# Performance work log

Hardware: AMD Instinct MI355X
Metric: run time of the kernel (lower is better)

Reference implementation:

```python
import jax, jax.numpy as jnp
import numpy as np

D_MODEL = 768
N_HEADS = 12
HEAD_DIM = D_MODEL // N_HEADS
D_FF = 3072
LN_EPS = 1e-12


def layer_norm(x, gamma, beta, eps=LN_EPS):
    mu = jnp.mean(x, axis=-1, keepdims=True)
    var = jnp.var(x, axis=-1, keepdims=True)
    return (x - mu) * jax.lax.rsqrt(var + eps) * gamma + beta


def setup_inputs() -> dict:
    key = jax.random.key(0)
    ks = jax.random.split(key, 16)
    B, S = 4, 2048
    p = lambda k, shape: (jax.random.normal(k, shape, dtype=jnp.float32) * 0.02)
    return {
        "hidden_states": jax.random.normal(ks[0], (B, S, D_MODEL), dtype=jnp.float32),
        "Wq": p(ks[1], (D_MODEL, D_MODEL)), "bq": jnp.zeros((D_MODEL,), jnp.float32),
        "Wk": p(ks[2], (D_MODEL, D_MODEL)), "bk": jnp.zeros((D_MODEL,), jnp.float32),
        "Wv": p(ks[3], (D_MODEL, D_MODEL)), "bv": jnp.zeros((D_MODEL,), jnp.float32),
        "Wo": p(ks[4], (D_MODEL, D_MODEL)), "bo": jnp.zeros((D_MODEL,), jnp.float32),
        "ln1_g": jnp.ones((D_MODEL,), jnp.float32), "ln1_b": jnp.zeros((D_MODEL,), jnp.float32),
        "Wi": p(ks[5], (D_FF, D_MODEL)), "bi": jnp.zeros((D_FF,), jnp.float32),
        "Wf": p(ks[6], (D_MODEL, D_FF)), "bf": jnp.zeros((D_MODEL,), jnp.float32),
        "ln2_g": jnp.ones((D_MODEL,), jnp.float32), "ln2_b": jnp.zeros((D_MODEL,), jnp.float32),
    }


def reference(hidden_states, Wq, bq, Wk, bk, Wv, bv, Wo, bo, ln1_g, ln1_b,
              Wi, bi, Wf, bf, ln2_g, ln2_b):
    B, S, _ = hidden_states.shape
    # Q/K/V projections (computed as in source; outputs then overwritten by constants)
    q = hidden_states @ Wq.T + bq
    k = hidden_states @ Wk.T + bk
    v = hidden_states @ Wv.T + bv
    split = lambda x: x.reshape(B, S, N_HEADS, HEAD_DIM).transpose(0, 2, 1, 3)
    q, k, v = split(q), split(k), split(v)
    # source: torch.full_like(..., 0.01) overwrite of q/k/v
    q = jnp.full_like(q, 0.01)
    k = jnp.full_like(k, 0.01)
    v = jnp.full_like(v, 0.01)
    # naive attention: full [B,H,S,S] score matrix materialized
    scores = jnp.einsum("bhqd,bhkd->bhqk", q, k) / jnp.sqrt(jnp.float32(HEAD_DIM))
    probs = jax.nn.softmax(scores, axis=-1)
    ctx = jnp.einsum("bhqk,bhkd->bhqd", probs, v)
    ctx = ctx.transpose(0, 2, 1, 3).reshape(B, S, D_MODEL)
    # self-output: dense + residual + LayerNorm (dropout is identity in eval)
    attn_out = layer_norm(ctx @ Wo.T + bo + hidden_states, ln1_g, ln1_b)
    # FFN: fc1 + exact GELU, fc2 + residual + LayerNorm
    h = jax.nn.gelu(attn_out @ Wi.T + bi, approximate=False)
    layer_out = layer_norm(h @ Wf.T + bf + attn_out, ln2_g, ln2_b)
    return layer_out
```

## Files before the change

kernel.cpp:

```cpp
#include <hip/hip_runtime.h>
#include <hip/hip_bf16.h>
#include <cstdint>
#include <cstddef>


typedef __bf16 bf16;
typedef __attribute__((ext_vector_type(8))) __bf16 bf16x8;
typedef __attribute__((ext_vector_type(4))) __bf16 bf16x4;
typedef __attribute__((ext_vector_type(4))) float floatx4;

#define DM    768
#define DF    3072
#define MROWS 8192

#define N8          (DF * DM / 8)
#define CONV_BLOCKS (2 * N8 / 256)
#define CVEC_BLOCKS (DM / 4)

__device__ __forceinline__ void gl2lds16(const void* gp, void* lp) {
  __builtin_amdgcn_global_load_lds(
      (__attribute__((address_space(1))) void*)(void*)gp,
      (__attribute__((address_space(3))) void*)lp,
      16, 0, 0);
}

__device__ __forceinline__ float gelu_fast(float x) {
  float x2 = x * x;
  float m  = x * __builtin_fmaf(-0.1029641f, x2, -2.3025851f);
  float e  = __builtin_amdgcn_exp2f(m);
  return x * __builtin_amdgcn_rcpf(1.0f + e);
}

__global__ __launch_bounds__(256)
void prep_kernel(const float* __restrict__ Wi, const float* __restrict__ Wf,
                 bf16* __restrict__ Wib, bf16* __restrict__ Wfb,
                 const float* __restrict__ Wo, const float* __restrict__ bo,
                 float* __restrict__ cvec) {
  if (blockIdx.x < CONV_BLOCKS) {
    int i = blockIdx.x * 256 + threadIdx.x;
    const float* src = (i < N8) ? Wi : Wf;
    bf16* dst        = (i < N8) ? Wib : Wfb;
    int k            = (i < N8) ? i : i - N8;
    const float4* p = (const float4*)(src + (size_t)k * 8);
    float4 x = p[0], y = p[1];
    bf16x8 o;
    o[0]=(bf16)x.x; o[1]=(bf16)x.y; o[2]=(bf16)x.z; o[3]=(bf16)x.w;
    o[4]=(bf16)y.x; o[5]=(bf16)y.y; o[6]=(bf16)y.z; o[7]=(bf16)y.w;
    *(bf16x8*)(dst + (size_t)k * 8) = o;
  } else {
    int row  = (blockIdx.x - CONV_BLOCKS) * 4 + (threadIdx.x >> 6);
    int lane = threadIdx.x & 63;
    const float4* r = (const float4*)(Wo + (size_t)row * DM);
    float s = 0.f;
    #pragma unroll
    for (int t = 0; t < 3; ++t) {
      float4 v = r[lane + t * 64];
      s += v.x + v.y + v.z + v.w;
    }
    #pragma unroll
    for (int o = 32; o > 0; o >>= 1) s += __shfl_xor(s, o);
    if (lane == 0) cvec[row] = 0.01f * s + bo[row];
  }
}

__global__ __launch_bounds__(256)
void ln1_kernel(const float* __restrict__ hid, const float* __restrict__ cvec,
                const float* __restrict__ g, const float* __restrict__ b,
                bf16* __restrict__ out) {
  int row  = blockIdx.x * 4 + (threadIdx.x >> 6);
  int lane = threadIdx.x & 63;
  const float4* hrow = (const float4*)(hid + (size_t)row * DM);
  const float4* cv4  = (const float4*)cvec;
  float x[12];
  float s = 0.f, sq = 0.f;
  #pragma unroll
  for (int t = 0; t < 3; ++t) {
    int c = lane + t * 64;
    float4 v = hrow[c];
    float4 cc = cv4[c];
    float x0 = v.x + cc.x, x1 = v.y + cc.y, x2 = v.z + cc.z, x3 = v.w + cc.w;
    x[t*4+0] = x0; x[t*4+1] = x1; x[t*4+2] = x2; x[t*4+3] = x3;
    s  += x0 + x1 + x2 + x3;
    sq += x0*x0 + x1*x1 + x2*x2 + x3*x3;
  }
  #pragma unroll
  for (int o = 32; o > 0; o >>= 1) { s += __shfl_xor(s, o); sq += __shfl_xor(sq, o); }
  float mu  = s * (1.0f / DM);
  float var = sq * (1.0f / DM) - mu * mu;
  float inv = rsqrtf(var + 1e-12f);
  const float4* g4 = (const float4*)g;
  const float4* b4 = (const float4*)b;
  #pragma unroll
  for (int t = 0; t < 3; ++t) {
    int c = lane + t * 64;
    float4 gg = g4[c], bb = b4[c];
    bf16x4 o4;
    o4[0] = (bf16)((x[t*4+0] - mu) * inv * gg.x + bb.x);
    o4[1] = (bf16)((x[t*4+1] - mu) * inv * gg.y + bb.y);
    o4[2] = (bf16)((x[t*4+2] - mu) * inv * gg.z + bb.z);
    o4[3] = (bf16)((x[t*4+3] - mu) * inv * gg.w + bb.w);
    *(bf16x4*)(out + (size_t)row * DM + c * 4) = o4;
  }
}

__global__ __launch_bounds__(256)
void ln2_kernel(const bf16* __restrict__ p0, const bf16* __restrict__ p1,
                const float* __restrict__ bias, const bf16* __restrict__ attn,
                const float* __restrict__ g, const float* __restrict__ b,
                float* __restrict__ out) {
  int row  = blockIdx.x * 4 + (threadIdx.x >> 6);
  int lane = threadIdx.x & 63;
  const bf16* r0 = p0 + (size_t)row * DM;
  const bf16* r1 = p1 + (size_t)row * DM;
  const bf16* ar = attn + (size_t)row * DM;
  const float4* bi4 = (const float4*)bias;
  float x[12];
  float s = 0.f, sq = 0.f;
  #pragma unroll
  for (int t = 0; t < 3; ++t) {
    int c = lane + t * 64;
    bf16x4 a = *(const bf16x4*)(r0 + c * 4);
    bf16x4 d = *(const bf16x4*)(r1 + c * 4);
    bf16x4 rv = *(const bf16x4*)(ar + c * 4);
    float4 bb = bi4[c];
    float x0 = (float)a[0] + (float)d[0] + bb.x + (float)rv[0];
    float x1 = (float)a[1] + (float)d[1] + bb.y + (float)rv[1];
    float x2 = (float)a[2] + (float)d[2] + bb.z + (float)rv[2];
    float x3 = (float)a[3] + (float)d[3] + bb.w + (float)rv[3];
    x[t*4+0] = x0; x[t*4+1] = x1; x[t*4+2] = x2; x[t*4+3] = x3;
    s  += x0 + x1 + x2 + x3;
    sq += x0*x0 + x1*x1 + x2*x2 + x3*x3;
  }
  #pragma unroll
  for (int o = 32; o > 0; o >>= 1) { s += __shfl_xor(s, o); sq += __shfl_xor(sq, o); }
  float mu  = s * (1.0f / DM);
  float var = sq * (1.0f / DM) - mu * mu;
  float inv = rsqrtf(var + 1e-12f);
  const float4* g4 = (const float4*)g;
  const float4* b4 = (const float4*)b;
  float4* orow = (float4*)(out + (size_t)row * DM);
  #pragma unroll
  for (int t = 0; t < 3; ++t) {
    int c = lane + t * 64;
    float4 gg = g4[c], bb = b4[c];
    float4 o;
    o.x = (x[t*4+0] - mu) * inv * gg.x + bb.x;
    o.y = (x[t*4+1] - mu) * inv * gg.y + bb.y;
    o.z = (x[t*4+2] - mu) * inv * gg.z + bb.z;
    o.w = (x[t*4+3] - mu) * inv * gg.w + bb.w;
    orow[c] = o;
  }
}

#define BM 128
#define BN 128
#define BK 64
#define ES 136

template <int EPI>
__global__ __launch_bounds__(256)
void gemm_nt(const bf16* __restrict__ A, const bf16* __restrict__ B,
             const float* __restrict__ bias,
             bf16* __restrict__ out, int M, int N, int K, int ksplit) {
  __shared__ __align__(16) unsigned char smem[BM * ES * 2];
  bf16* lds_a = (bf16*)smem;
  bf16* lds_b = lds_a + BM * BK;

  const int tid   = threadIdx.x;
  const int wave  = tid >> 6;
  const int lane  = tid & 63;
  const int quad  = lane >> 4;
  const int row16 = lane & 15;
  const int xorv  = row16 & 7;

  const int m0 = blockIdx.y * BM;
  const int n0 = blockIdx.x * BN;
  const int wm = (wave >> 1) * 64;
  const int wn = (wave & 1) * 64;

  const int kbeg = blockIdx.z * ksplit;
  const int kend = kbeg + ksplit;

  floatx4 acc[4][4] = {};

  const bf16* Ablk = A + (size_t)m0 * K;
  const bf16* Bblk = B + (size_t)n0 * K;

  for (int kk = kbeg; kk < kend; kk += BK) {
    #pragma unroll
    for (int i = 0; i < 4; ++i) {
      int ci  = tid + 256 * i;
      int r   = ci >> 3;
      int c_g = (ci & 7) ^ (r & 7);
      gl2lds16(Ablk + (size_t)r * K + kk + c_g * 8, lds_a + ci * 8);
      gl2lds16(Bblk + (size_t)r * K + kk + c_g * 8, lds_b + ci * 8);
    }
    __syncthreads();

    #pragma unroll
    for (int ks = 0; ks < BK; ks += 32) {
      const int cs = ((ks >> 3) + quad) ^ xorv;
      bf16x8 af[4], bfr[4];
      #pragma unroll
      for (int i = 0; i < 4; ++i)
        af[i] = *(const bf16x8*)&lds_a[(wm + i * 16 + row16) * BK + cs * 8];
      #pragma unroll
      for (int j = 0; j < 4; ++j)
        bfr[j] = *(const bf16x8*)&lds_b[(wn + j * 16 + row16) * BK + cs * 8];
      #pragma unroll
      for (int i = 0; i < 4; ++i)
        #pragma unroll
        for (int j = 0; j < 4; ++j)
          acc[i][j] = __builtin_amdgcn_mfma_f32_16x16x32_bf16(af[i], bfr[j], acc[i][j], 0, 0, 0);
    }
    __syncthreads();
  }

  bf16* eb = (bf16*)smem;

  float bia[4];
  if constexpr (EPI == 0) {
    #pragma unroll
    for (int j = 0; j < 4; ++j) bia[j] = bias[n0 + wn + j * 16 + row16];
  }

  #pragma unroll
  for (int i = 0; i < 4; ++i) {
    #pragma unroll
    for (int j = 0; j < 4; ++j) {
      int col = wn + j * 16 + row16;
      #pragma unroll
      for (int r = 0; r < 4; ++r) {
        int row = wm + i * 16 + quad * 4 + r;
        float x = acc[i][j][r];
        if constexpr (EPI == 0) x = gelu_fast(x + bia[j]);
        eb[row * ES + col] = (bf16)x;
      }
    }
  }
  __syncthreads();

  bf16* outp = out + (EPI == 1 ? (size_t)blockIdx.z * M * N : 0);
  const int rsub = tid >> 4;
  const int csub = (tid & 15) * 8;
  #pragma unroll
  for (int c = 0; c < 8; ++c) {
    int row = c * 16 + rsub;
    bf16x8 v = *(const bf16x8*)&eb[row * ES + csub];
    *(bf16x8*)&outp[(size_t)(m0 + row) * N + n0 + csub] = v;
  }
}

extern "C" void kernel_launch(void* const* d_in, const int* in_sizes, int n_in,
                              void* d_out, int out_size, void* d_ws, size_t ws_size,
                              hipStream_t stream) {
  (void)in_sizes; (void)n_in; (void)out_size; (void)ws_size;

  const float* hidden = (const float*)d_in[0];
  const float* Wo     = (const float*)d_in[7];
  const float* bo     = (const float*)d_in[8];
  const float* ln1_g  = (const float*)d_in[9];
  const float* ln1_b  = (const float*)d_in[10];
  const float* Wi     = (const float*)d_in[11];
  const float* bi     = (const float*)d_in[12];
  const float* Wf     = (const float*)d_in[13];
  const float* bf_    = (const float*)d_in[14];
  const float* ln2_g  = (const float*)d_in[15];
  const float* ln2_b  = (const float*)d_in[16];
  float* out = (float*)d_out;

  char* w = (char*)d_ws;
  float* cvec = (float*)w;
  size_t off = 4096;
  bf16* attn = (bf16*)(w + off); off += (size_t)MROWS * DM * 2;
  bf16* h    = (bf16*)(w + off); off += (size_t)MROWS * DF * 2;
  bf16* pre  = (bf16*)(w + off); off += (size_t)2 * MROWS * DM * 2;
  bf16* Wib  = (bf16*)(w + off); off += (size_t)DF * DM * 2;
  bf16* Wfb  = (bf16*)(w + off);

  prep_kernel<<<dim3(CONV_BLOCKS + CVEC_BLOCKS), dim3(256), 0, stream>>>(
      Wi, Wf, Wib, Wfb, Wo, bo, cvec);

  ln1_kernel<<<dim3(MROWS / 4), dim3(256), 0, stream>>>(hidden, cvec, ln1_g, ln1_b, attn);

  gemm_nt<0><<<dim3(DF / BN, MROWS / BM, 1), dim3(256), 0, stream>>>(
      attn, Wib, bi, h, MROWS, DF, DM, DM);

  gemm_nt<1><<<dim3(DM / BN, MROWS / BM, 2), dim3(256), 0, stream>>>(
      h, Wfb, nullptr, pre, MROWS, DM, DF, DF / 2);

  ln2_kernel<<<dim3(MROWS / 4), dim3(256), 0, stream>>>(
      pre, pre + (size_t)MROWS * DM, bf_, attn, ln2_g, ln2_b, out);
}
```

Measured before the change: 238.4 us.

## Fuse LayerNorm2 into split-K FC2 GEMM via last-block atomic election

Removes the separate ln2 kernel launch. Each FC2 GEMM block writes its bf16 partial tile and increments a per-row-block atomic counter. The block that sees the final count (12 tiles: 6 N-tiles times 2 K-splits) then runs LayerNorm over that 128-row slab. The counter is zeroed in the prep kernel. This saves a launch and lets the LN overlap with GEMM tail work, but the LN is now serialized onto one block per row slab, which may leave CUs idle at the end.

```diff
diff --git a/kernel.cpp b/kernel.cpp
--- a/kernel.cpp
+++ b/kernel.cpp
@@ -35,7 +35,7 @@
 void prep_kernel(const float* __restrict__ Wi, const float* __restrict__ Wf,
                  bf16* __restrict__ Wib, bf16* __restrict__ Wfb,
                  const float* __restrict__ Wo, const float* __restrict__ bo,
-                 float* __restrict__ cvec) {
+                 float* __restrict__ cvec, int* __restrict__ ctr) {
   if (blockIdx.x < CONV_BLOCKS) {
     int i = blockIdx.x * 256 + threadIdx.x;
     const float* src = (i < N8) ? Wi : Wf;
@@ -48,6 +48,8 @@
     o[4]=(bf16)y.x; o[5]=(bf16)y.y; o[6]=(bf16)y.z; o[7]=(bf16)y.w;
     *(bf16x8*)(dst + (size_t)k * 8) = o;
   } else {
+    if (blockIdx.x == CONV_BLOCKS && threadIdx.x < 64)
+      ctr[threadIdx.x] = 0;
     int row  = (blockIdx.x - CONV_BLOCKS) * 4 + (threadIdx.x >> 6);
     int lane = threadIdx.x & 63;
     const float4* r = (const float4*)(Wo + (size_t)row * DM);
@@ -103,65 +105,15 @@
   }
 }
 
-__global__ __launch_bounds__(256)
-void ln2_kernel(const bf16* __restrict__ p0, const bf16* __restrict__ p1,
-                const float* __restrict__ bias, const bf16* __restrict__ attn,
-                const float* __restrict__ g, const float* __restrict__ b,
-                float* __restrict__ out) {
-  int row  = blockIdx.x * 4 + (threadIdx.x >> 6);
-  int lane = threadIdx.x & 63;
-  const bf16* r0 = p0 + (size_t)row * DM;
-  const bf16* r1 = p1 + (size_t)row * DM;
-  const bf16* ar = attn + (size_t)row * DM;
-  const float4* bi4 = (const float4*)bias;
-  float x[12];
-  float s = 0.f, sq = 0.f;
-  #pragma unroll
-  for (int t = 0; t < 3; ++t) {
-    int c = lane + t * 64;
-    bf16x4 a = *(const bf16x4*)(r0 + c * 4);
-    bf16x4 d = *(const bf16x4*)(r1 + c * 4);
-    bf16x4 rv = *(const bf16x4*)(ar + c * 4);
-    float4 bb = bi4[c];
-    float x0 = (float)a[0] + (float)d[0] + bb.x + (float)rv[0];
-    float x1 = (float)a[1] + (float)d[1] + bb.y + (float)rv[1];
-    float x2 = (float)a[2] + (float)d[2] + bb.z + (float)rv[2];
-    float x3 = (float)a[3] + (float)d[3] + bb.w + (float)rv[3];
-    x[t*4+0] = x0; x[t*4+1] = x1; x[t*4+2] = x2; x[t*4+3] = x3;
-    s  += x0 + x1 + x2 + x3;
-    sq += x0*x0 + x1*x1 + x2*x2 + x3*x3;
-  }
-  #pragma unroll
-  for (int o = 32; o > 0; o >>= 1) { s += __shfl_xor(s, o); sq += __shfl_xor(sq, o); }
-  float mu  = s * (1.0f / DM);
-  float var = sq * (1.0f / DM) - mu * mu;
-  float inv = rsqrtf(var + 1e-12f);
-  const float4* g4 = (const float4*)g;
-  const float4* b4 = (const float4*)b;
-  float4* orow = (float4*)(out + (size_t)row * DM);
-  #pragma unroll
-  for (int t = 0; t < 3; ++t) {
-    int c = lane + t * 64;
-    float4 gg = g4[c], bb = b4[c];
-    float4 o;
-    o.x = (x[t*4+0] - mu) * inv * gg.x + bb.x;
-    o.y = (x[t*4+1] - mu) * inv * gg.y + bb.y;
-    o.z = (x[t*4+2] - mu) * inv * gg.z + bb.z;
-    o.w = (x[t*4+3] - mu) * inv * gg.w + bb.w;
-    orow[c] = o;
-  }
-}
-
 #define BM 128
 #define BN 128
 #define BK 64
 #define ES 136
 
-template <int EPI>
 __global__ __launch_bounds__(256)
-void gemm_nt(const bf16* __restrict__ A, const bf16* __restrict__ B,
-             const float* __restrict__ bias,
-             bf16* __restrict__ out, int M, int N, int K, int ksplit) {
+void gemm1(const bf16* __restrict__ A, const bf16* __restrict__ B,
+           const float* __restrict__ bias, bf16* __restrict__ out,
+           int M, int N, int K) {
   __shared__ __align__(16) unsigned char smem[BM * ES * 2];
   bf16* lds_a = (bf16*)smem;
   bf16* lds_b = lds_a + BM * BK;
@@ -178,15 +130,11 @@
   const int wm = (wave >> 1) * 64;
   const int wn = (wave & 1) * 64;
 
-  const int kbeg = blockIdx.z * ksplit;
-  const int kend = kbeg + ksplit;
-
   floatx4 acc[4][4] = {};
-
   const bf16* Ablk = A + (size_t)m0 * K;
   const bf16* Bblk = B + (size_t)n0 * K;
 
-  for (int kk = kbeg; kk < kend; kk += BK) {
+  for (int kk = 0; kk < K; kk += BK) {
     #pragma unroll
     for (int i = 0; i < 4; ++i) {
       int ci  = tid + 256 * i;
@@ -196,7 +144,6 @@
       gl2lds16(Bblk + (size_t)r * K + kk + c_g * 8, lds_b + ci * 8);
     }
     __syncthreads();
-
     #pragma unroll
     for (int ks = 0; ks < BK; ks += 32) {
       const int cs = ((ks >> 3) + quad) ^ xorv;
@@ -217,30 +164,106 @@
   }
 
   bf16* eb = (bf16*)smem;
-
   float bia[4];
-  if constexpr (EPI == 0) {
-    #pragma unroll
-    for (int j = 0; j < 4; ++j) bia[j] = bias[n0 + wn + j * 16 + row16];
-  }
-
-  #pragma unroll
-  for (int i = 0; i < 4; ++i) {
+  #pragma unroll
+  for (int j = 0; j < 4; ++j) bia[j] = bias[n0 + wn + j * 16 + row16];
+
+  #pragma unroll
+  for (int i = 0; i < 4; ++i)
     #pragma unroll
     for (int j = 0; j < 4; ++j) {
       int col = wn + j * 16 + row16;
       #pragma unroll
       for (int r = 0; r < 4; ++r) {
         int row = wm + i * 16 + quad * 4 + r;
-        float x = acc[i][j][r];
-        if constexpr (EPI == 0) x = gelu_fast(x + bia[j]);
-        eb[row * ES + col] = (bf16)x;
+        eb[row * ES + col] = (bf16)gelu_fast(acc[i][j][r] + bia[j]);
       }
     }
-  }
   __syncthreads();
 
-  bf16* outp = out + (EPI == 1 ? (size_t)blockIdx.z * M * N : 0);
+  const int rsub = tid >> 4;
+  const int csub = (tid & 15) * 8;
+  #pragma unroll
+  for (int c = 0; c < 8; ++c) {
+    int row = c * 16 + rsub;
+    bf16x8 v = *(const bf16x8*)&eb[row * ES + csub];
+    *(bf16x8*)&out[(size_t)(m0 + row) * N + n0 + csub] = v;
+  }
+}
+
+__global__ __launch_bounds__(256)
+void gemm2_ln(const bf16* __restrict__ A, const bf16* __restrict__ B,
+              bf16* __restrict__ partial, const bf16* __restrict__ attn,
+              const float* __restrict__ bias,
+              const float* __restrict__ g, const float* __restrict__ b,
+              float* __restrict__ out, int* __restrict__ ctr) {
+  const int M = MROWS, N = DM, K = DF;
+  __shared__ __align__(16) unsigned char smem[BM * ES * 2];
+  bf16* lds_a = (bf16*)smem;
+  bf16* lds_b = lds_a + BM * BK;
+
+  const int tid   = threadIdx.x;
+  const int wave  = tid >> 6;
+  const int lane  = tid & 63;
+  const int quad  = lane >> 4;
+  const int row16 = lane & 15;
+  const int xorv  = row16 & 7;
+
+  const int m0 = blockIdx.y * BM;
+  const int n0 = blockIdx.x * BN;
+  const int wm = (wave >> 1) * 64;
+  const int wn = (wave & 1) * 64;
+  const int kbeg = blockIdx.z * (K / 2);
+  const int kend = kbeg + K / 2;
+
+  floatx4 acc[4][4] = {};
+  const bf16* Ablk = A + (size_t)m0 * K;
+  const bf16* Bblk = B + (size_t)n0 * K;
+
+  for (int kk = kbeg; kk < kend; kk += BK) {
+    #pragma unroll
+    for (int i = 0; i < 4; ++i) {
+      int ci  = tid + 256 * i;
+      int r   = ci >> 3;
+      int c_g = (ci & 7) ^ (r & 7);
+      gl2lds16(Ablk + (size_t)r * K + kk + c_g * 8, lds_a + ci * 8);
+      gl2lds16(Bblk + (size_t)r * K + kk + c_g * 8, lds_b + ci * 8);
+    }
+    __syncthreads();
+    #pragma unroll
+    for (int ks = 0; ks < BK; ks += 32) {
+      const int cs = ((ks >> 3) + quad) ^ xorv;
+      bf16x8 af[4], bfr[4];
+      #pragma unroll
+      for (int i = 0; i < 4; ++i)
+        af[i] = *(const bf16x8*)&lds_a[(wm + i * 16 + row16) * BK + cs * 8];
+      #pragma unroll
+      for (int j = 0; j < 4; ++j)
+        bfr[j] = *(const bf16x8*)&lds_b[(wn + j * 16 + row16) * BK + cs * 8];
+      #pragma unroll
+      for (int i = 0; i < 4; ++i)
+        #pragma unroll
+        for (int j = 0; j < 4; ++j)
+          acc[i][j] = __builtin_amdgcn_mfma_f32_16x16x32_bf16(af[i], bfr[j], acc[i][j], 0, 0, 0);
+    }
+    __syncthreads();
+  }
+
+  bf16* eb = (bf16*)smem;
+  #pragma unroll
+  for (int i = 0; i < 4; ++i)
+    #pragma unroll
+    for (int j = 0; j < 4; ++j) {
+      int col = wn + j * 16 + row16;
+      #pragma unroll
+      for (int r = 0; r < 4; ++r) {
+        int row = wm + i * 16 + quad * 4 + r;
+        eb[row * ES + col] = (bf16)acc[i][j][r];
+      }
+    }
+  __syncthreads();
+
+  bf16* outp = partial + (size_t)blockIdx.z * M * N;
   const int rsub = tid >> 4;
   const int csub = (tid & 15) * 8;
   #pragma unroll
@@ -248,6 +271,60 @@
     int row = c * 16 + rsub;
     bf16x8 v = *(const bf16x8*)&eb[row * ES + csub];
     *(bf16x8*)&outp[(size_t)(m0 + row) * N + n0 + csub] = v;
+  }
+
+  __threadfence();
+  __shared__ int elect;
+  if (tid == 0) elect = atomicAdd(&ctr[blockIdx.y], 1);
+  __syncthreads();
+  if (elect != 11) return;
+  __threadfence();
+
+  const bf16* p0 = partial;
+  const bf16* p1 = partial + (size_t)M * N;
+  const float4* bi4 = (const float4*)bias;
+  const float4* g4  = (const float4*)g;
+  const float4* b4  = (const float4*)b;
+
+  for (int rr = wave; rr < BM; rr += 4) {
+    int row = m0 + rr;
+    const bf16* r0 = p0 + (size_t)row * DM;
+    const bf16* r1 = p1 + (size_t)row * DM;
+    const bf16* ar = attn + (size_t)row * DM;
+    float x[12];
+    float s = 0.f, sq = 0.f;
+    #pragma unroll
+    for (int t = 0; t < 3; ++t) {
+      int c = lane + t * 64;
+      bf16x4 a  = *(const bf16x4*)(r0 + c * 4);
+      bf16x4 d  = *(const bf16x4*)(r1 + c * 4);
+      bf16x4 rv = *(const bf16x4*)(ar + c * 4);
+      float4 bb = bi4[c];
+      float x0 = (float)a[0] + (float)d[0] + bb.x + (float)rv[0];
+      float x1 = (float)a[1] + (float)d[1] + bb.y + (float)rv[1];
+      float x2 = (float)a[2] + (float)d[2] + bb.z + (float)rv[2];
+      float x3 = (float)a[3] + (float)d[3] + bb.w + (float)rv[3];
+      x[t*4+0] = x0; x[t*4+1] = x1; x[t*4+2] = x2; x[t*4+3] = x3;
+      s  += x0 + x1 + x2 + x3;
+      sq += x0*x0 + x1*x1 + x2*x2 + x3*x3;
+    }
+    #pragma unroll
+    for (int o = 32; o > 0; o >>= 1) { s += __shfl_xor(s, o); sq += __shfl_xor(sq, o); }
+    float mu  = s * (1.0f / DM);
+    float var = sq * (1.0f / DM) - mu * mu;
+    float inv = rsqrtf(var + 1e-12f);
+    float4* orow = (float4*)(out + (size_t)row * DM);
+    #pragma unroll
+    for (int t = 0; t < 3; ++t) {
+      int c = lane + t * 64;
+      float4 gg = g4[c], bb = b4[c];
+      float4 o;
+      o.x = (x[t*4+0] - mu) * inv * gg.x + bb.x;
+      o.y = (x[t*4+1] - mu) * inv * gg.y + bb.y;
+      o.z = (x[t*4+2] - mu) * inv * gg.z + bb.z;
+      o.w = (x[t*4+3] - mu) * inv * gg.w + bb.w;
+      orow[c] = o;
+    }
   }
 }
 
@@ -271,6 +348,7 @@
 
   char* w = (char*)d_ws;
   float* cvec = (float*)w;
+  int*   ctr  = (int*)(w + 3072);
   size_t off = 4096;
   bf16* attn = (bf16*)(w + off); off += (size_t)MROWS * DM * 2;
   bf16* h    = (bf16*)(w + off); off += (size_t)MROWS * DF * 2;
@@ -279,16 +357,13 @@
   bf16* Wfb  = (bf16*)(w + off);
 
   prep_kernel<<<dim3(CONV_BLOCKS + CVEC_BLOCKS), dim3(256), 0, stream>>>(
-      Wi, Wf, Wib, Wfb, Wo, bo, cvec);
+      Wi, Wf, Wib, Wfb, Wo, bo, cvec, ctr);
 
   ln1_kernel<<<dim3(MROWS / 4), dim3(256), 0, stream>>>(hidden, cvec, ln1_g, ln1_b, attn);
 
-  gemm_nt<0><<<dim3(DF / BN, MROWS / BM, 1), dim3(256), 0, stream>>>(
-      attn, Wib, bi, h, MROWS, DF, DM, DM);
-
-  gemm_nt<1><<<dim3(DM / BN, MROWS / BM, 2), dim3(256), 0, stream>>>(
-      h, Wfb, nullptr, pre, MROWS, DM, DF, DF / 2);
-
-  ln2_kernel<<<dim3(MROWS / 4), dim3(256), 0, stream>>>(
-      pre, pre + (size_t)MROWS * DM, bf_, attn, ln2_g, ln2_b, out);
-}
+  gemm1<<<dim3(DF / BN, MROWS / BM), dim3(256), 0, stream>>>(
+      attn, Wib, bi, h, MROWS, DF, DM);
+
+  gemm2_ln<<<dim3(DM / BN, MROWS / BM, 2), dim3(256), 0, stream>>>(
+      h, Wfb, pre, attn, bf_, ln2_g, ln2_b, out, ctr);
+}
```

After: 399.7 us. +67.6%, slower.
